# Performance work log

Hardware: AMD Instinct MI355X
Metric: run time of the kernel (lower is better)

Reference implementation:

```python
import jax, jax.numpy as jnp
import numpy as np

DIM = 768; NL = 13; NH = 12; VOCAB = 50257; SEQ = 512; B = 4
HID = 4 * DIM; HD = DIM // NH; LUT_SIZE = 256


def setup_inputs() -> dict:
    key = jax.random.key(0)
    ks = jax.random.split(key, 10)
    def n(k, shape, s=0.02):
        return jax.random.normal(k, shape, jnp.float32) * s
    return {
        'lut': jnp.linspace(-0.1, 0.1, LUT_SIZE, dtype=jnp.float32),  # 256-entry primal codebook
        'tok_emb': n(ks[0], (VOCAB, DIM)),
        'pos_emb': n(ks[1], (SEQ, DIM)),
        'ln1_g': jnp.ones((NL, DIM), jnp.float32), 'ln1_b': jnp.zeros((NL, DIM), jnp.float32),
        'in_w': n(ks[2], (NL, 3 * DIM, DIM)), 'in_b': jnp.zeros((NL, 3 * DIM), jnp.float32),
        'out_w': n(ks[3], (NL, DIM, DIM)), 'out_b': jnp.zeros((NL, DIM), jnp.float32),
        'ln2_g': jnp.ones((NL, DIM), jnp.float32), 'ln2_b': jnp.zeros((NL, DIM), jnp.float32),
        'mlp1_scale': jnp.ones((NL, HID, 1), jnp.float32),
        'mlp2_scale': jnp.ones((NL, DIM, 1), jnp.float32),
        'lnf_g': jnp.ones((DIM,), jnp.float32), 'lnf_b': jnp.zeros((DIM,), jnp.float32),
        'head_scale': jnp.ones((VOCAB, 1), jnp.float32),
        'mlp1_idx': jax.random.randint(ks[4], (NL, HID, DIM), 0, LUT_SIZE, jnp.int32),
        'mlp2_idx': jax.random.randint(ks[5], (NL, DIM, HID), 0, LUT_SIZE, jnp.int32),
        'head_idx': jax.random.randint(ks[6], (VOCAB, DIM), 0, LUT_SIZE, jnp.int32),
        'idx': jax.random.randint(ks[7], (B, SEQ), 0, VOCAB, jnp.int32),
    }


def layernorm(x, g, b, eps=1e-5):
    m = jnp.mean(x, -1, keepdims=True)
    v = jnp.var(x, -1, keepdims=True)
    return (x - m) * jax.lax.rsqrt(v + eps) * g + b


def ghost_linear(x, gidx, scale, lut):
    # dequantize: gather codebook values, row-scale, then matmul (no bias)
    w = lut[gidx] * scale  # [out, in]
    return x @ w.T


def mha(x, wi, bi, wo, bo, mask):
    Bn, T, D = x.shape
    qkv = x @ wi.T + bi
    q, k, v = jnp.split(qkv, 3, axis=-1)
    q = q.reshape(Bn, T, NH, HD); k = k.reshape(Bn, T, NH, HD); v = v.reshape(Bn, T, NH, HD)
    s = jnp.einsum('bqhd,bkhd->bhqk', q, k) / jnp.sqrt(jnp.float32(HD)) + mask
    a = jax.nn.softmax(s, axis=-1)
    o = jnp.einsum('bhqk,bkhd->bqhd', a, v).reshape(Bn, T, D)
    return o @ wo.T + bo


def reference(lut, tok_emb, pos_emb, ln1_g, ln1_b, in_w, in_b, out_w, out_b,
              ln2_g, ln2_b, mlp1_scale, mlp2_scale, lnf_g, lnf_b, head_scale,
              mlp1_idx, mlp2_idx, head_idx, idx):
    Bn, T = idx.shape
    x = tok_emb[idx] + pos_emb[:T]
    causal = jnp.triu(jnp.ones((T, T), bool), 1)
    mask = jnp.where(causal, -jnp.inf, 0.0).astype(jnp.float32)
    for l in range(NL):
        h = layernorm(x, ln1_g[l], ln1_b[l])
        x = x + mha(h, in_w[l], in_b[l], out_w[l], out_b[l], mask)
        h = layernorm(x, ln2_g[l], ln2_b[l])
        h = ghost_linear(h, mlp1_idx[l], mlp1_scale[l], lut)
        h = jax.nn.gelu(h, approximate=True)  # GELU tanh approximation
        x = x + ghost_linear(h, mlp2_idx[l], mlp2_scale[l], lut)
    x = layernorm(x, lnf_g, lnf_b)
    return ghost_linear(x, head_idx, head_scale, lut)
```

## Files before the change

### kernel.cpp

```cpp
#include <hip/hip_runtime.h>
#include <stdint.h>

#define DIM 768
#define NL 13
#define NH 12
#define VOCAB 50257
#define SEQ 512
#define BATCH 4
#define HID 3072
#define HD 64
#define NTOK (BATCH*SEQ)
#define BHB (BATCH*NH)

typedef unsigned short u16;
typedef __attribute__((ext_vector_type(8))) __bf16 bf16x8;
typedef __attribute__((ext_vector_type(4))) float f32x4;

__device__ __forceinline__ u16 f2bf(float f) {
    union { float f; uint32_t u; } v; v.f = f;
    uint32_t u = v.u;
    return (u16)((u + 0x7FFFu + ((u >> 16) & 1u)) >> 16);
}

__device__ __forceinline__ void gl2lds16(const void* g, void* l) {
    __builtin_amdgcn_global_load_lds((const __attribute__((address_space(1))) void*)g,
                                     (__attribute__((address_space(3))) void*)l,
                                     16, 0, 0);
}

__device__ __forceinline__ float gelu_tanh(float x) {
    float x3 = x * x * x;
    float t = tanhf(0.7978845608028654f * (x + 0.044715f * x3));
    return 0.5f * x * (1.0f + t);
}

__device__ __forceinline__ void xcd_remap(int& bx, int& by) {
    const int gx = gridDim.x;
    const int nwg = gx * gridDim.y;
    const int orig = by * gx + bx;
    const int xcd = orig & 7;
    const int q = nwg >> 3, r = nwg & 7;
    const int wg = (xcd < r ? xcd * (q + 1) : r * (q + 1) + (xcd - r) * q) + (orig >> 3);
    bx = wg % gx; by = wg / gx;
}

template<int EPI>
__device__ __forceinline__ void epi_store(float v, int r, int c, int N, int z, long sC,
                                          const float* bias, const float* resid,
                                          void* out0, void* out1, void* out2)
{
    if constexpr (EPI == 0) {
        if (c < N) ((float*)out0)[(long)z * sC + (long)r * N + c] = v;
    } else if constexpr (EPI == 1) {
        v += bias[c];
        const int part = c / DIM;
        const int cc = c - part * DIM;
        const int hh = cc >> 6, d = cc & 63;
        const int b = r >> 9, t = r & 511;
        const int bh = b * NH + hh;
        if (part == 0)      ((u16*)out0)[((long)bh * SEQ + t) * HD + d] = f2bf(v);
        else if (part == 1) ((u16*)out1)[((long)bh * SEQ + t) * HD + d] = f2bf(v);
        else                ((u16*)out2)[((long)bh * HD + d) * SEQ + t] = f2bf(v);
    } else if constexpr (EPI == 3) {
        if (bias) v += bias[c];
        v += resid[(long)r * N + c];
        ((float*)out0)[(long)r * N + c] = v;
    } else {
        ((u16*)out0)[(long)r * N + c] = f2bf(gelu_tanh(v));
    }
}

template<int WN, int EPI>
__global__ __launch_bounds__(256, 2)
void gemm_bt(const u16* __restrict__ A, const u16* __restrict__ B,
             const float* __restrict__ bias, const float* __restrict__ resid,
             void* __restrict__ out0, void* __restrict__ out1, void* __restrict__ out2,
             int M, int N, int K, long sA, long sB, long sC)
{
    constexpr int TN = WN * 32;
    constexpr int NBG = TN / 64;
    __shared__ __align__(16) u16 As[2 * 128 * 32];
    __shared__ __align__(16) u16 Bs[2 * TN * 32];

    const int tid  = threadIdx.x;
    const int wave = tid >> 6;
    const int lane = tid & 63;
    const int quad = lane >> 4;
    const int l16  = lane & 15;
    const int wm   = wave >> 1;
    const int wn   = wave & 1;

    int bx = blockIdx.x, by = blockIdx.y;
    xcd_remap(bx, by);

    const int m0 = bx * 128;
    const int n0 = by * TN;
    const int z  = blockIdx.z;

    const u16* Ab = A + (long)z * sA;
    const u16* Bb = B + (long)z * sB;

    const int srow = tid >> 2;
    const int scol = ((tid & 3) ^ ((srow >> 1) & 3)) * 8;

    const long aoff0 = (long)(m0 + srow) * K + scol;
    const long aoff1 = (long)(m0 + 64 + srow) * K + scol;
    long boff[NBG];
    #pragma unroll
    for (int g = 0; g < NBG; g++) {
        int br = n0 + g * 64 + srow; if (br > N - 1) br = N - 1;
        boff[g] = (long)br * K + scol;
    }

    auto stage = [&](int b, int k0) {
        gl2lds16(Ab + aoff0 + k0, As + b * 4096 + wave * 512);
        gl2lds16(Ab + aoff1 + k0, As + b * 4096 + 2048 + wave * 512);
        #pragma unroll
        for (int g = 0; g < NBG; g++)
            gl2lds16(Bb + boff[g] + k0, Bs + b * (TN * 32) + g * 2048 + wave * 512);
    };

    f32x4 acc[4][WN];
    #pragma unroll
    for (int i = 0; i < 4; i++)
        #pragma unroll
        for (int j = 0; j < WN; j++)
            acc[i][j] = (f32x4){0.f, 0.f, 0.f, 0.f};

    const int sq8 = (quad ^ ((l16 >> 1) & 3)) * 8;
    const int arow = (wm * 64 + l16) * 32 + sq8;
    const int brow = (wn * (WN * 16) + l16) * 32 + sq8;

    stage(0, 0);
    __syncthreads();

    int cur = 0;
    for (int k0 = 0; k0 < K; k0 += 32) {
        if (k0 + 32 < K) stage(cur ^ 1, k0 + 32);

        const u16* Ar = As + cur * 4096;
        const u16* Br = Bs + cur * (TN * 32);
        bf16x8 af[4], bfr[WN];
        #pragma unroll
        for (int i = 0; i < 4; i++)
            af[i] = *(const bf16x8*)&Ar[arow + i * 512];
        #pragma unroll
        for (int j = 0; j < WN; j++)
            bfr[j] = *(const bf16x8*)&Br[brow + j * 512];
        #pragma unroll
        for (int i = 0; i < 4; i++)
            #pragma unroll
            for (int j = 0; j < WN; j++)
                acc[i][j] = __builtin_amdgcn_mfma_f32_16x16x32_bf16(af[i], bfr[j], acc[i][j], 0, 0, 0);

        __syncthreads();
        cur ^= 1;
    }

    const int rbase = m0 + wm * 64;
    const int cbase = n0 + wn * (WN * 16);
    #pragma unroll
    for (int i = 0; i < 4; i++)
        #pragma unroll
        for (int j = 0; j < WN; j++)
            #pragma unroll
            for (int rg = 0; rg < 4; rg++)
                epi_store<EPI>(acc[i][j][rg], rbase + i * 16 + quad * 4 + rg,
                               cbase + j * 16 + l16, N, z, sC, bias, resid, out0, out1, out2);
}

template<int WN, int EPI>
__global__ __launch_bounds__(256)
void gemm64(const u16* __restrict__ A, const u16* __restrict__ B,
            const float* __restrict__ bias, const float* __restrict__ resid,
            void* __restrict__ out0, void* __restrict__ out1, void* __restrict__ out2,
            int M, int N, int K)
{
    constexpr int TN = WN * 32;
    constexpr int NC = TN / 32;
    __shared__ __align__(16) u16 As[2 * 64 * 64];
    __shared__ __align__(16) u16 Bs[2 * TN * 64];

    const int tid  = threadIdx.x;
    const int wave = tid >> 6;
    const int lane = tid & 63;
    const int quad = lane >> 4;
    const int l16  = lane & 15;
    const int wm   = wave >> 1;
    const int wn   = wave & 1;

    int bx = blockIdx.x, by = blockIdx.y;
    xcd_remap(bx, by);
    const int m0 = bx * 64;
    const int n0 = by * TN;

    const int srow = tid >> 3;
    const int sch  = ((tid & 7) ^ (srow & 7)) * 8;
    u16* const asw = As + wave * 512;
    u16* const bsw = Bs + wave * 512;

    const long aoff = (long)(m0 + srow) * K + sch;
    const long boff = (long)(n0 + srow) * K + sch;

    auto stageA = [&](int b, int k0) {
        #pragma unroll
        for (int c = 0; c < 2; c++)
            gl2lds16(A + aoff + (long)c * 32 * K + k0, asw + b * 4096 + c * 2048);
    };
    auto stageB = [&](int b, int k0) {
        #pragma unroll
        for (int c = 0; c < NC; c++)
            gl2lds16(B + boff + (long)c * 32 * K + k0, bsw + b * TN * 64 + c * 2048);
    };

    f32x4 acc[2][WN];
    #pragma unroll
    for (int i = 0; i < 2; i++)
        #pragma unroll
        for (int j = 0; j < WN; j++)
            acc[i][j] = (f32x4){0.f, 0.f, 0.f, 0.f};

    const int rsw = l16 & 7;

    stageA(0, 0);
    stageB(0, 0);
    __syncthreads();

    int cur = 0;
    for (int k0 = 0; k0 < K; k0 += 64) {
        const bool more = (k0 + 64 < K);
        if (more) {
            stageA(cur ^ 1, k0 + 64);
            stageB(cur ^ 1, k0 + 64);
        }

        const u16* Ar = As + cur * 4096;
        const u16* Br = Bs + cur * TN * 64;
        bf16x8 af[2][2], bfr[WN][2];
        #pragma unroll
        for (int i = 0; i < 2; i++)
            #pragma unroll
            for (int kk = 0; kk < 2; kk++)
                af[i][kk] = *(const bf16x8*)&Ar[(wm * 32 + i * 16 + l16) * 64 + (((kk * 4 + quad) ^ rsw) * 8)];
        #pragma unroll
        for (int j = 0; j < WN; j++)
            #pragma unroll
            for (int kk = 0; kk < 2; kk++)
                bfr[j][kk] = *(const bf16x8*)&Br[(wn * (WN * 16) + j * 16 + l16) * 64 + (((kk * 4 + quad) ^ rsw) * 8)];
        #pragma unroll
        for (int kk = 0; kk < 2; kk++)
            #pragma unroll
            for (int i = 0; i < 2; i++)
                #pragma unroll
                for (int j = 0; j < WN; j++)
                    acc[i][j] = __builtin_amdgcn_mfma_f32_16x16x32_bf16(af[i][kk], bfr[j][kk], acc[i][j], 0, 0, 0);

        __syncthreads();
        cur ^= 1;
    }

    const int rbase = m0 + wm * 32;
    const int cbase = n0 + wn * (WN * 16);
    #pragma unroll
    for (int i = 0; i < 2; i++)
        #pragma unroll
        for (int j = 0; j < WN; j++)
            #pragma unroll
            for (int rg = 0; rg < 4; rg++)
                epi_store<EPI>(acc[i][j][rg], rbase + i * 16 + quad * 4 + rg,
                               cbase + j * 16 + l16, N, 0, 0, bias, resid, out0, out1, out2);
}

__global__ __launch_bounds__(256)
void attn_kernel(const u16* __restrict__ qb, const u16* __restrict__ kb,
                 const u16* __restrict__ vtb, u16* __restrict__ ob)
{
    __shared__ __align__(16) u16 Ks[512 * 64];
    __shared__ __align__(16) u16 Vs[64 * 512];
    __shared__ __align__(16) u16 Ps[4][32 * 64];

    const int tid  = threadIdx.x;
    const int wave = tid >> 6;
    const int lane = tid & 63;
    const int quad = lane >> 4;
    const int l16  = lane & 15;

    const int bh   = blockIdx.x;
    const int qblk = blockIdx.y;
    const int qr0  = qblk * 128 + wave * 32;

    #pragma unroll 4
    for (int cI = 0; cI < 16; ++cI) {
        const int rbase = cI * 32 + wave * 8;
        const int r  = rbase + (lane >> 3);
        const int ch = lane & 7;
        gl2lds16(kb + ((long)bh * SEQ + r) * HD + ((ch ^ (r & 7)) * 8), Ks + rbase * 64);
    }
    #pragma unroll 4
    for (int cI = 0; cI < 16; ++cI) {
        const int d = cI * 4 + wave;
        gl2lds16(vtb + ((long)bh * HD + d) * SEQ + ((lane ^ (d & 7)) * 8), Vs + d * 512);
    }

    bf16x8 af[2][2];
    const long qoff = ((long)bh * SEQ + qr0) * HD;
    #pragma unroll
    for (int i = 0; i < 2; i++)
        #pragma unroll
        for (int kc = 0; kc < 2; kc++)
            af[i][kc] = *(const bf16x8*)&qb[qoff + (long)(i * 16 + l16) * HD + kc * 32 + quad * 8];

    __syncthreads();

    f32x4 o[2][4];
    float mrun[2][4], lrun[2][4];
    #pragma unroll
    for (int i = 0; i < 2; i++)
        #pragma unroll
        for (int rg = 0; rg < 4; rg++) { mrun[i][rg] = -1e30f; lrun[i][rg] = 0.f; }
    #pragma unroll
    for (int i = 0; i < 2; i++)
        #pragma unroll
        for (int nd = 0; nd < 4; nd++)
            o[i][nd] = (f32x4){0.f, 0.f, 0.f, 0.f};

    u16* const Pw = &Ps[wave][0];
    const int rsw = l16 & 7;
    const int kvend = qr0 + 32;

    for (int kv0 = 0; kv0 < kvend; kv0 += 64) {
        f32x4 s[2][4];
        #pragma unroll
        for (int i = 0; i < 2; i++)
            #pragma unroll
            for (int n = 0; n < 4; n++)
                s[i][n] = (f32x4){0.f, 0.f, 0.f, 0.f};
        bf16x8 bf[4][2];
        #pragma unroll
        for (int n = 0; n < 4; n++)
            #pragma unroll
            for (int kc = 0; kc < 2; kc++)
                bf[n][kc] = *(const bf16x8*)&Ks[(kv0 + n * 16 + l16) * 64 + (((kc * 4 + quad) ^ rsw) * 8)];
        #pragma unroll
        for (int i = 0; i < 2; i++)
            #pragma unroll
            for (int n = 0; n < 4; n++)
                #pragma unroll
                for (int kc = 0; kc < 2; kc++)
                    s[i][n] = __builtin_amdgcn_mfma_f32_16x16x32_bf16(af[i][kc], bf[n][kc], s[i][n], 0, 0, 0);

        #pragma unroll
        for (int i = 0; i < 2; i++) {
            #pragma unroll
            for (int rg = 0; rg < 4; rg++) {
                const int q = qr0 + i * 16 + quad * 4 + rg;
                float v[4];
                #pragma unroll
                for (int n = 0; n < 4; n++) {
                    const int c = kv0 + n * 16 + l16;
                    v[n] = (c <= q) ? s[i][n][rg] * 0.125f : -1e30f;
                }
                float pm = fmaxf(fmaxf(v[0], v[1]), fmaxf(v[2], v[3]));
                #pragma unroll
                for (int off = 1; off < 16; off <<= 1) pm = fmaxf(pm, __shfl_xor(pm, off));
                const float mo = mrun[i][rg];
                const float mn = fmaxf(mo, pm);
                const float corr = __expf(mo - mn);
                float ps = 0.f;
                #pragma unroll
                for (int n = 0; n < 4; n++) { const float e = __expf(v[n] - mn); v[n] = e; ps += e; }
                #pragma unroll
                for (int off = 1; off < 16; off <<= 1) ps += __shfl_xor(ps, off);
                lrun[i][rg] = lrun[i][rg] * corr + ps;
                mrun[i][rg] = mn;
                #pragma unroll
                for (int nd = 0; nd < 4; nd++) o[i][nd][rg] *= corr;
                const int qlz = i * 16 + quad * 4 + rg;
                const int sw = qlz & 7;
                #pragma unroll
                for (int n = 0; n < 4; n++)
                    Pw[qlz * 64 + (((n * 2 + (l16 >> 3)) ^ sw) * 8) + (l16 & 7)] = f2bf(v[n]);
            }
        }
        asm volatile("s_waitcnt lgkmcnt(0)" ::: "memory");

        bf16x8 pa[2][2], vb[4][2];
        #pragma unroll
        for (int i = 0; i < 2; i++)
            #pragma unroll
            for (int kc = 0; kc < 2; kc++)
                pa[i][kc] = *(const bf16x8*)&Pw[(i * 16 + l16) * 64 + (((kc * 4 + quad) ^ rsw) * 8)];
        #pragma unroll
        for (int nd = 0; nd < 4; nd++)
            #pragma unroll
            for (int kc = 0; kc < 2; kc++)
                vb[nd][kc] = *(const bf16x8*)&Vs[(nd * 16 + l16) * 512 + ((((kv0 >> 3) + kc * 4 + quad) ^ rsw) * 8)];
        #pragma unroll
        for (int i = 0; i < 2; i++)
            #pragma unroll
            for (int nd = 0; nd < 4; nd++)
                #pragma unroll
                for (int kc = 0; kc < 2; kc++)
                    o[i][nd] = __builtin_amdgcn_mfma_f32_16x16x32_bf16(pa[i][kc], vb[nd][kc], o[i][nd], 0, 0, 0);
    }

    const int b  = bh / NH, hh = bh - b * NH;
    #pragma unroll
    for (int i = 0; i < 2; i++) {
        #pragma unroll
        for (int rg = 0; rg < 4; rg++) {
            const float inv = 1.f / lrun[i][rg];
            const int t = qr0 + i * 16 + quad * 4 + rg;
            u16* orow = ob + ((long)(b * SEQ + t)) * DIM + hh * HD;
            #pragma unroll
            for (int nd = 0; nd < 4; nd++)
                orow[nd * 16 + l16] = f2bf(o[i][nd][rg] * inv);
        }
    }
}

__global__ __launch_bounds__(256)
void embed_kernel(const int* __restrict__ tokidx, const float* __restrict__ tok,
                  const float* __restrict__ pos, float* __restrict__ x)
{
    const int i = blockIdx.x * 256 + threadIdx.x;
    const int row = i / 192;
    const int c4 = i - row * 192;
    const int t = row & (SEQ - 1);
    const int tk = tokidx[row];
    const float4 a = *(const float4*)&tok[(long)tk * DIM + c4 * 4];
    const float4 p = *(const float4*)&pos[(long)t * DIM + c4 * 4];
    *(float4*)&x[(long)row * DIM + c4 * 4] = make_float4(a.x + p.x, a.y + p.y, a.z + p.z, a.w + p.w);
}

__global__ __launch_bounds__(256)
void ln_kernel(const float* __restrict__ x, const float* __restrict__ g,
               const float* __restrict__ b, u16* __restrict__ out)
{
    const int row = blockIdx.x * 4 + (threadIdx.x >> 6);
    const int lane = threadIdx.x & 63;
    const float* xr = x + (long)row * DIM;
    float v[12];
    float s = 0.f, s2 = 0.f;
    #pragma unroll
    for (int i = 0; i < 3; i++) {
        const float4 f = *(const float4*)&xr[i * 256 + lane * 4];
        v[i*4+0] = f.x; v[i*4+1] = f.y; v[i*4+2] = f.z; v[i*4+3] = f.w;
        s  += f.x + f.y + f.z + f.w;
        s2 += f.x*f.x + f.y*f.y + f.z*f.z + f.w*f.w;
    }
    for (int o = 32; o; o >>= 1) { s += __shfl_xor(s, o); s2 += __shfl_xor(s2, o); }
    const float m  = s * (1.f / DIM);
    const float var = s2 * (1.f / DIM) - m * m;
    const float rs = rsqrtf(var + 1e-5f);
    u16* orow = out + (long)row * DIM;
    #pragma unroll
    for (int i = 0; i < 3; i++) {
        const int c = i * 256 + lane * 4;
        ushort4 o4 = make_ushort4(
            f2bf((v[i*4+0] - m) * rs * g[c+0] + b[c+0]),
            f2bf((v[i*4+1] - m) * rs * g[c+1] + b[c+1]),
            f2bf((v[i*4+2] - m) * rs * g[c+2] + b[c+2]),
            f2bf((v[i*4+3] - m) * rs * g[c+3] + b[c+3]));
        *(ushort4*)&orow[c] = o4;
    }
}

__global__ __launch_bounds__(256)
void tobf16_kernel(const float* __restrict__ in, u16* __restrict__ out)
{
    const long i = ((long)blockIdx.x * 256 + threadIdx.x) * 4;
    const float4 f = *(const float4*)&in[i];
    *(ushort4*)&out[i] = make_ushort4(f2bf(f.x), f2bf(f.y), f2bf(f.z), f2bf(f.w));
}

__global__ __launch_bounds__(256)
void dequant_kernel(const int* __restrict__ gidx, const float* __restrict__ scale,
                    const float* __restrict__ lut, u16* __restrict__ w,
                    long total, int Kd)
{
    __shared__ float slut[256];
    slut[threadIdx.x] = lut[threadIdx.x];
    __syncthreads();
    const long i4 = ((long)blockIdx.x * 256 + threadIdx.x) * 4;
    if (i4 >= total) return;
    const int4 g = *(const int4*)&gidx[i4];
    const float sc = scale[(int)(i4 / Kd)];
    *(ushort4*)&w[i4] = make_ushort4(f2bf(slut[g.x] * sc), f2bf(slut[g.y] * sc),
                                     f2bf(slut[g.z] * sc), f2bf(slut[g.w] * sc));
}

extern "C" void kernel_launch(void* const* d_in, const int* in_sizes, int n_in,
                              void* d_out, int out_size, void* d_ws, size_t ws_size,
                              hipStream_t stream)
{
    const float* lut        = (const float*)d_in[0];
    const float* tok_emb    = (const float*)d_in[1];
    const float* pos_emb    = (const float*)d_in[2];
    const float* ln1_g      = (const float*)d_in[3];
    const float* ln1_b      = (const float*)d_in[4];
    const float* in_w       = (const float*)d_in[5];
    const float* in_b       = (const float*)d_in[6];
    const float* out_w      = (const float*)d_in[7];
    const float* out_b      = (const float*)d_in[8];
    const float* ln2_g      = (const float*)d_in[9];
    const float* ln2_b      = (const float*)d_in[10];
    const float* mlp1_scale = (const float*)d_in[11];
    const float* mlp2_scale = (const float*)d_in[12];
    const float* lnf_g      = (const float*)d_in[13];
    const float* lnf_b      = (const float*)d_in[14];
    const float* head_scale = (const float*)d_in[15];
    const int*   mlp1_idx   = (const int*)d_in[16];
    const int*   mlp2_idx   = (const int*)d_in[17];
    const int*   head_idx   = (const int*)d_in[18];
    const int*   tokids     = (const int*)d_in[19];

    char* p = (char*)d_ws;
    auto alloc = [&](size_t bytes) { char* r = p; p += (bytes + 255) & ~(size_t)255; return r; };
    float* x    = (float*)alloc((size_t)NTOK * DIM * 4);
    u16*  h     = (u16*) alloc((size_t)NTOK * DIM * 2);
    u16*  h2    = (u16*) alloc((size_t)NTOK * HID * 2);
    u16*  qb    = (u16*) alloc((size_t)BHB * SEQ * HD * 2);
    u16*  kb    = (u16*) alloc((size_t)BHB * SEQ * HD * 2);
    u16*  vtb   = (u16*) alloc((size_t)BHB * SEQ * HD * 2);
    u16*  ob    = (u16*) alloc((size_t)NTOK * DIM * 2);
    u16*  inw16 = (u16*) alloc((size_t)NL * 3 * DIM * DIM * 2);
    u16*  outw16= (u16*) alloc((size_t)NL * DIM * DIM * 2);
    u16*  w1    = (u16*) alloc((size_t)HID * DIM * 2);
    u16*  w2    = (u16*) alloc((size_t)DIM * HID * 2);
    u16*  hw    = (u16*) alloc((size_t)VOCAB * DIM * 2);

    embed_kernel<<<NTOK * 192 / 256, 256, 0, stream>>>(tokids, tok_emb, pos_emb, x);
    tobf16_kernel<<<NL * 3 * DIM * DIM / 1024, 256, 0, stream>>>(in_w, inw16);
    tobf16_kernel<<<NL * DIM * DIM / 1024, 256, 0, stream>>>(out_w, outw16);
    {
        const long total = (long)VOCAB * DIM;
        const int blocks = (int)((total / 4 + 255) / 256);
        dequant_kernel<<<blocks, 256, 0, stream>>>(head_idx, head_scale, lut, hw, total, DIM);
    }

    for (int l = 0; l < NL; l++) {
        ln_kernel<<<NTOK / 4, 256, 0, stream>>>(x, ln1_g + l * DIM, ln1_b + l * DIM, h);
        gemm64<4, 1><<<dim3(NTOK / 64, 3 * DIM / 128), 256, 0, stream>>>(
            h, inw16 + (long)l * 3 * DIM * DIM, in_b + l * 3 * DIM, nullptr,
            qb, kb, vtb, NTOK, 3 * DIM, DIM);
        attn_kernel<<<dim3(BHB, 4), 256, 0, stream>>>(qb, kb, vtb, ob);
        gemm64<2, 3><<<dim3(NTOK / 64, DIM / 64), 256, 0, stream>>>(
            ob, outw16 + (long)l * DIM * DIM, out_b + l * DIM, x,
            x, nullptr, nullptr, NTOK, DIM, DIM);
        ln_kernel<<<NTOK / 4, 256, 0, stream>>>(x, ln2_g + l * DIM, ln2_b + l * DIM, h);
        dequant_kernel<<<HID * DIM / 1024, 256, 0, stream>>>(
            mlp1_idx + (long)l * HID * DIM, mlp1_scale + l * HID, lut, w1, (long)HID * DIM, DIM);
        gemm64<4, 4><<<dim3(NTOK / 64, HID / 128), 256, 0, stream>>>(
            h, w1, nullptr, nullptr, h2, nullptr, nullptr, NTOK, HID, DIM);
        dequant_kernel<<<DIM * HID / 1024, 256, 0, stream>>>(
            mlp2_idx + (long)l * DIM * HID, mlp2_scale + l * DIM, lut, w2, (long)DIM * HID, HID);
        gemm64<2, 3><<<dim3(NTOK / 64, DIM / 64), 256, 0, stream>>>(
            h2, w2, nullptr, x, x, nullptr, nullptr, NTOK, DIM, HID);
    }

    ln_kernel<<<NTOK / 4, 256, 0, stream>>>(x, lnf_g, lnf_b, h);
    gemm_bt<8, 0><<<dim3(NTOK / 128, (VOCAB + 255) / 256, 1), 256, 0, stream>>>(
        h, hw, nullptr, nullptr, d_out, nullptr, nullptr, NTOK, VOCAB, DIM, 0, 0, 0);
}
```

Before: 2.808 ms.

## Hoist MLP dequant out of layer loop, split-K MLP2 with atomics, retile head GEMM

When the workspace is large enough, all layers' MLP weights are dequantized up front in two large launches instead of two per layer. The MLP2 down-projection now splits K into two halves across blockIdx.z and accumulates into the residual with float atomicAdd, which doubles grid parallelism but makes the summation order nondeterministic. The LM head GEMM switches from 256-wide to 128-wide N tiles and drops the two-blocks-per-SM launch bound. These are independent tweaks aimed at launch overhead, occupancy and tile balance.

Result: faster. 2.638 ms (-6.0%).

```diff
diff --git a/kernel.cpp b/kernel.cpp
--- a/kernel.cpp
+++ b/kernel.cpp
@@ -65,13 +65,15 @@
         if (bias) v += bias[c];
         v += resid[(long)r * N + c];
         ((float*)out0)[(long)r * N + c] = v;
+    } else if constexpr (EPI == 5) {
+        atomicAdd(&((float*)out0)[(long)r * N + c], v);
     } else {
         ((u16*)out0)[(long)r * N + c] = f2bf(gelu_tanh(v));
     }
 }
 
 template<int WN, int EPI>
-__global__ __launch_bounds__(256, 2)
+__global__ __launch_bounds__(256)
 void gemm_bt(const u16* __restrict__ A, const u16* __restrict__ B,
              const float* __restrict__ bias, const float* __restrict__ resid,
              void* __restrict__ out0, void* __restrict__ out1, void* __restrict__ out2,
@@ -174,7 +176,7 @@
 void gemm64(const u16* __restrict__ A, const u16* __restrict__ B,
             const float* __restrict__ bias, const float* __restrict__ resid,
             void* __restrict__ out0, void* __restrict__ out1, void* __restrict__ out2,
-            int M, int N, int K)
+            int M, int N, int K, int Kstride)
 {
     constexpr int TN = WN * 32;
     constexpr int NC = TN / 32;
@@ -193,24 +195,25 @@
     xcd_remap(bx, by);
     const int m0 = bx * 64;
     const int n0 = by * TN;
+    const int koff = blockIdx.z * K;
 
     const int srow = tid >> 3;
     const int sch  = ((tid & 7) ^ (srow & 7)) * 8;
     u16* const asw = As + wave * 512;
     u16* const bsw = Bs + wave * 512;
 
-    const long aoff = (long)(m0 + srow) * K + sch;
-    const long boff = (long)(n0 + srow) * K + sch;
+    const long aoff = (long)(m0 + srow) * Kstride + koff + sch;
+    const long boff = (long)(n0 + srow) * Kstride + koff + sch;
 
     auto stageA = [&](int b, int k0) {
         #pragma unroll
         for (int c = 0; c < 2; c++)
-            gl2lds16(A + aoff + (long)c * 32 * K + k0, asw + b * 4096 + c * 2048);
+            gl2lds16(A + aoff + (long)c * 32 * Kstride + k0, asw + b * 4096 + c * 2048);
     };
     auto stageB = [&](int b, int k0) {
         #pragma unroll
         for (int c = 0; c < NC; c++)
-            gl2lds16(B + boff + (long)c * 32 * K + k0, bsw + b * TN * 64 + c * 2048);
+            gl2lds16(B + boff + (long)c * 32 * Kstride + k0, bsw + b * TN * 64 + c * 2048);
     };
 
     f32x4 acc[2][WN];
@@ -526,9 +529,13 @@
     u16*  ob    = (u16*) alloc((size_t)NTOK * DIM * 2);
     u16*  inw16 = (u16*) alloc((size_t)NL * 3 * DIM * DIM * 2);
     u16*  outw16= (u16*) alloc((size_t)NL * DIM * DIM * 2);
-    u16*  w1    = (u16*) alloc((size_t)HID * DIM * 2);
-    u16*  w2    = (u16*) alloc((size_t)DIM * HID * 2);
     u16*  hw    = (u16*) alloc((size_t)VOCAB * DIM * 2);
+
+    const size_t layerW = (size_t)HID * DIM * 2;
+    const size_t used   = (size_t)(p - (char*)d_ws);
+    const bool hoist    = ws_size >= used + 2 * NL * layerW + 1024;
+    u16* w1 = (u16*)alloc(hoist ? NL * layerW : layerW);
+    u16* w2 = (u16*)alloc(hoist ? NL * layerW : layerW);
 
     embed_kernel<<<NTOK * 192 / 256, 256, 0, stream>>>(tokids, tok_emb, pos_emb, x);
     tobf16_kernel<<<NL * 3 * DIM * DIM / 1024, 256, 0, stream>>>(in_w, inw16);
@@ -538,28 +545,38 @@
         const int blocks = (int)((total / 4 + 255) / 256);
         dequant_kernel<<<blocks, 256, 0, stream>>>(head_idx, head_scale, lut, hw, total, DIM);
     }
+    if (hoist) {
+        const long t1 = (long)NL * HID * DIM;
+        dequant_kernel<<<(int)(t1 / 1024), 256, 0, stream>>>(mlp1_idx, mlp1_scale, lut, w1, t1, DIM);
+        dequant_kernel<<<(int)(t1 / 1024), 256, 0, stream>>>(mlp2_idx, mlp2_scale, lut, w2, t1, HID);
+    }
 
     for (int l = 0; l < NL; l++) {
+        u16* w1l = hoist ? w1 + (size_t)l * HID * DIM : w1;
+        u16* w2l = hoist ? w2 + (size_t)l * HID * DIM : w2;
+
         ln_kernel<<<NTOK / 4, 256, 0, stream>>>(x, ln1_g + l * DIM, ln1_b + l * DIM, h);
         gemm64<4, 1><<<dim3(NTOK / 64, 3 * DIM / 128), 256, 0, stream>>>(
             h, inw16 + (long)l * 3 * DIM * DIM, in_b + l * 3 * DIM, nullptr,
-            qb, kb, vtb, NTOK, 3 * DIM, DIM);
+            qb, kb, vtb, NTOK, 3 * DIM, DIM, DIM);
         attn_kernel<<<dim3(BHB, 4), 256, 0, stream>>>(qb, kb, vtb, ob);
         gemm64<2, 3><<<dim3(NTOK / 64, DIM / 64), 256, 0, stream>>>(
             ob, outw16 + (long)l * DIM * DIM, out_b + l * DIM, x,
-            x, nullptr, nullptr, NTOK, DIM, DIM);
+            x, nullptr, nullptr, NTOK, DIM, DIM, DIM);
         ln_kernel<<<NTOK / 4, 256, 0, stream>>>(x, ln2_g + l * DIM, ln2_b + l * DIM, h);
-        dequant_kernel<<<HID * DIM / 1024, 256, 0, stream>>>(
-            mlp1_idx + (long)l * HID * DIM, mlp1_scale + l * HID, lut, w1, (long)HID * DIM, DIM);
+        if (!hoist)
+            dequant_kernel<<<HID * DIM / 1024, 256, 0, stream>>>(
+                mlp1_idx + (long)l * HID * DIM, mlp1_scale + l * HID, lut, w1l, (long)HID * DIM, DIM);
         gemm64<4, 4><<<dim3(NTOK / 64, HID / 128), 256, 0, stream>>>(
-            h, w1, nullptr, nullptr, h2, nullptr, nullptr, NTOK, HID, DIM);
-        dequant_kernel<<<DIM * HID / 1024, 256, 0, stream>>>(
-            mlp2_idx + (long)l * DIM * HID, mlp2_scale + l * DIM, lut, w2, (long)DIM * HID, HID);
-        gemm64<2, 3><<<dim3(NTOK / 64, DIM / 64), 256, 0, stream>>>(
-            h2, w2, nullptr, x, x, nullptr, nullptr, NTOK, DIM, HID);
+            h, w1l, nullptr, nullptr, h2, nullptr, nullptr, NTOK, HID, DIM, DIM);
+        if (!hoist)
+            dequant_kernel<<<DIM * HID / 1024, 256, 0, stream>>>(
+                mlp2_idx + (long)l * DIM * HID, mlp2_scale + l * DIM, lut, w2l, (long)DIM * HID, HID);
+        gemm64<2, 5><<<dim3(NTOK / 64, DIM / 64, 2), 256, 0, stream>>>(
+            h2, w2l, nullptr, nullptr, x, nullptr, nullptr, NTOK, DIM, HID / 2, HID);
     }
 
     ln_kernel<<<NTOK / 4, 256, 0, stream>>>(x, lnf_g, lnf_b, h);
-    gemm_bt<8, 0><<<dim3(NTOK / 128, (VOCAB + 255) / 256, 1), 256, 0, stream>>>(
+    gemm_bt<4, 0><<<dim3(NTOK / 128, (VOCAB + 127) / 128, 1), 256, 0, stream>>>(
         h, hw, nullptr, nullptr, d_out, nullptr, nullptr, NTOK, VOCAB, DIM, 0, 0, 0);
 }
```
